# Kernel tuning notes

Hardware: AMD Instinct MI355X
Metric: run time of the kernel (lower is better)

Reference implementation:

```python
import jax, jax.numpy as jnp
import numpy as np

VOCAB = 50257
EMB = 512


def setup_inputs() -> dict:
    key = jax.random.key(0)
    k1, k2, k3 = jax.random.split(key, 3)
    input_token_ids = jax.random.randint(k1, (8, 4096), 0, VOCAB, dtype=jnp.int64 if jax.config.jax_enable_x64 else jnp.int32)
    W = jax.random.normal(k2, (EMB, VOCAB), dtype=jnp.float32)  # nn.Linear(vocab, emb).weight
    b = jax.random.normal(k3, (EMB,), dtype=jnp.float32)        # nn.Linear bias
    return {"input_token_ids": input_token_ids, "W": W, "b": b}


def reference(input_token_ids, W, b):
    # one_hot(ids, V) @ W.T + b  ==  W.T[ids] + b   (exact same math, gather form)
    scale = jnp.asarray(EMB, W.dtype) ** 0.5
    emb = jnp.take(W.T, input_token_ids, axis=0)  # [B, S, EMB]
    return (emb + b) * scale
```

## Files before the change

kernel.cpp:

```cpp
#include <hip/hip_runtime.h>


constexpr int VOCAB = 50257;
constexpr int EMB   = 512;
constexpr int NTOK  = 8 * 4096;
constexpr float SCALE = 22.62741699796952f;

constexpr int VB   = 64;
constexpr int NB   = (VOCAB + VB - 1) / VB;
constexpr int CAP  = 96;
constexpr int ESPL = 4;
constexpr int RWV  = 32;
constexpr int RS   = VB + 1;


__global__ __launch_bounds__(256) void build_buckets(
    const int* __restrict__ ids,
    int* __restrict__ counts,
    int* __restrict__ olist,
    int* __restrict__ buckets)
{
    int t = blockIdx.x * 256 + threadIdx.x;
    int id = ids[t];
    int bkt = id >> 6;
    int slot = atomicAdd(&counts[bkt], 1);
    if (slot < CAP) {
        buckets[bkt * CAP + slot] = (t << 6) | (id & 63);
    } else {
        int o = atomicAdd(&counts[NB], 1);
        olist[o] = t;
    }
}

__global__ __launch_bounds__(256) void scatter_main(
    const float* __restrict__ W,
    const float* __restrict__ bias,
    const int*   __restrict__ counts,
    const int*   __restrict__ buckets,
    const int*   __restrict__ olist,
    const int*   __restrict__ ids,
    float*       __restrict__ out)
{
    __shared__ float tile[4][RWV * RS];
    __shared__ int   toks[CAP];
    __shared__ int   s_cnt;

    const int bid  = blockIdx.x;
    const int b    = bid >> 2;
    const int z    = bid & 3;
    const int tid  = threadIdx.x;
    const int lane = tid & 63;
    const int w    = tid >> 6;

    if (tid == 0) s_cnt = counts[b];
    if (tid < CAP) toks[tid] = buckets[b * CAP + tid];
    __syncthreads();
    const int cnt = min(s_cnt, CAP);

    const int e0 = z * 128 + w * RWV;
    const int el = lane & 31;
    const float be = bias[e0 + el];

    const int v = b * VB + lane;
    const float* wsrc = W + (v < VOCAB ? v : VOCAB - 1);

    if (cnt > 0) {
        #pragma unroll
        for (int r = 0; r < RWV; ++r) {
            const float* gp = wsrc + (size_t)(e0 + r) * VOCAB;
            float* lp = &tile[w][r * RS];
            __builtin_amdgcn_global_load_lds(
                (const __attribute__((address_space(1))) void*)gp,
                (__attribute__((address_space(3))) void*)lp, 4, 0, 0);
        }
        asm volatile("s_waitcnt vmcnt(0)" ::: "memory");

        const int half = lane >> 5;
        const float* tw = &tile[w][el * RS];
        for (int i = 0; i < cnt; i += 2) {
            int j  = i + half;
            int jj = j < cnt ? j : cnt - 1;
            int pk = toks[jj];
            int t  = pk >> 6;
            int vl = pk & 63;
            float val = (tw[vl] + be) * SCALE;
            if (j < cnt) out[(size_t)t * EMB + e0 + el] = val;
        }
    }

    if (b == 0) {
        int n = counts[NB];
        for (int ww = w; ww < n; ww += 4) {
            int t  = olist[ww];
            int id = ids[t];
            #pragma unroll
            for (int m = 0; m < 2; ++m) {
                int e = z * 128 + lane + m * 64;
                out[(size_t)t * EMB + e] = (W[(size_t)e * VOCAB + id] + bias[e]) * SCALE;
            }
        }
    }
}

__global__ __launch_bounds__(256) void embed_gather(
    const int*   __restrict__ ids,
    const float* __restrict__ W,
    const float* __restrict__ b,
    float*       __restrict__ out)
{
    int idx4 = blockIdx.x * blockDim.x + threadIdx.x;
    int t    = idx4 >> 7;
    int e    = (idx4 & 127) << 2;
    int id = ids[t];
    float4 bb = *reinterpret_cast<const float4*>(b + e);
    const float* wcol = W + (size_t)id;
    float4 o;
    o.x = (wcol[(size_t)(e + 0) * VOCAB] + bb.x) * SCALE;
    o.y = (wcol[(size_t)(e + 1) * VOCAB] + bb.y) * SCALE;
    o.z = (wcol[(size_t)(e + 2) * VOCAB] + bb.z) * SCALE;
    o.w = (wcol[(size_t)(e + 3) * VOCAB] + bb.w) * SCALE;
    *reinterpret_cast<float4*>(out + (size_t)idx4 * 4) = o;
}

extern "C" void kernel_launch(void* const* d_in, const int* in_sizes, int n_in,
                              void* d_out, int out_size, void* d_ws, size_t ws_size,
                              hipStream_t stream)
{
    const int*   ids  = (const int*)  d_in[0];
    const float* W    = (const float*)d_in[1];
    const float* bias = (const float*)d_in[2];
    float*       out  = (float*)d_out;

    const size_t ws_ints_needed = (size_t)NB + 1 + NTOK + (size_t)NB * CAP;

    if (ws_size >= ws_ints_needed * sizeof(int)) {
        int* counts  = (int*)d_ws;
        int* olist   = counts + NB + 1;
        int* buckets = olist + NTOK;

        hipMemsetAsync(counts, 0, (NB + 1) * sizeof(int), stream);
        build_buckets<<<NTOK / 256, 256, 0, stream>>>(ids, counts, olist, buckets);
        scatter_main<<<NB * ESPL, 256, 0, stream>>>(W, bias, counts, buckets,
                                                    olist, ids, out);
    } else {
        constexpr int total4 = NTOK * EMB / 4;
        embed_gather<<<total4 / 256, 256, 0, stream>>>(ids, W, bias, out);
    }
}
```

Before: 195.9 us.

## Use 16-byte swizzled LDS loads and register-held token lists in scatter kernel

Rewrites the W tile staging in scatter_main to use 16-byte global_load_lds transfers from 4-aligned row segments into an XOR-swizzled LDS layout, plus a small tail buffer for the misaligned remainder. The per-block token list now lives in registers and is broadcast with readlane instead of going through shared memory and a __syncthreads. The output loop is unrolled four-wide so loads are batched before stores. This targets fewer load instructions and less sync overhead, at the cost of more complex and fragile indexing (alignment, vadj for the last bucket, and the tail path).

After: 196.4 us. No clear change (+0.3%).

```diff
diff --git a/kernel.cpp b/kernel.cpp
--- a/kernel.cpp
+++ b/kernel.cpp
@@ -11,7 +11,8 @@
 constexpr int CAP  = 96;
 constexpr int ESPL = 4;
 constexpr int RWV  = 32;
-constexpr int RS   = VB + 1;
+constexpr int MAIN_DW = RWV * 64;
+constexpr int TAIL_DW = RWV * 4;
 
 
 __global__ __launch_bounds__(256) void build_buckets(
@@ -41,9 +42,7 @@
     const int*   __restrict__ ids,
     float*       __restrict__ out)
 {
-    __shared__ float tile[4][RWV * RS];
-    __shared__ int   toks[CAP];
-    __shared__ int   s_cnt;
+    __shared__ float tile[4][MAIN_DW + TAIL_DW];
 
     const int bid  = blockIdx.x;
     const int b    = bid >> 2;
@@ -52,40 +51,78 @@
     const int lane = tid & 63;
     const int w    = tid >> 6;
 
-    if (tid == 0) s_cnt = counts[b];
-    if (tid < CAP) toks[tid] = buckets[b * CAP + tid];
-    __syncthreads();
-    const int cnt = min(s_cnt, CAP);
+    const int e0     = z * 128 + w * RWV;
+    const int vstart = min(b * VB, VOCAB - VB);
+    const int vadj   = b * VB - vstart;
 
-    const int e0 = z * 128 + w * RWV;
-    const int el = lane & 31;
-    const float be = bias[e0 + el];
+    int   cnt_v = counts[b];
+    int   tok_a = buckets[b * CAP + lane];
+    int   tok_b = buckets[b * CAP + 64 + (lane & 31)];
+    float be    = bias[e0 + (lane & 31)];
 
-    const int v = b * VB + lane;
-    const float* wsrc = W + (v < VOCAB ? v : VOCAB - 1);
-
-    if (cnt > 0) {
+    {
+        const int rl = lane >> 4;
+        const int p  = lane & 15;
         #pragma unroll
-        for (int r = 0; r < RWV; ++r) {
-            const float* gp = wsrc + (size_t)(e0 + r) * VOCAB;
-            float* lp = &tile[w][r * RS];
+        for (int i = 0; i < 8; ++i) {
+            const int r = 4 * i + rl;
+            const int q = p ^ (r & 15);
+            const size_t rowdw = (size_t)(e0 + r) * VOCAB + vstart;
+            const float* gp = W + ((rowdw & ~(size_t)3) + 4 * (size_t)q);
+            float* lp = &tile[w][i * 256];
+            __builtin_amdgcn_global_load_lds(
+                (const __attribute__((address_space(1))) void*)gp,
+                (__attribute__((address_space(3))) void*)lp, 16, 0, 0);
+        }
+        #pragma unroll
+        for (int j = 0; j < 2; ++j) {
+            const int f = 64 * j + lane;
+            const int r = f >> 2, d = f & 3;
+            const size_t rowdw = (size_t)(e0 + r) * VOCAB + vstart;
+            const float* gp = W + (rowdw + 60 + d);
+            float* lp = &tile[w][MAIN_DW + j * 64];
             __builtin_amdgcn_global_load_lds(
                 (const __attribute__((address_space(1))) void*)gp,
                 (__attribute__((address_space(3))) void*)lp, 4, 0, 0);
         }
-        asm volatile("s_waitcnt vmcnt(0)" ::: "memory");
+    }
 
-        const int half = lane >> 5;
-        const float* tw = &tile[w][el * RS];
-        for (int i = 0; i < cnt; i += 2) {
-            int j  = i + half;
-            int jj = j < cnt ? j : cnt - 1;
-            int pk = toks[jj];
-            int t  = pk >> 6;
-            int vl = pk & 63;
-            float val = (tw[vl] + be) * SCALE;
-            if (j < cnt) out[(size_t)t * EMB + e0 + el] = val;
+    const int cnt = min(__builtin_amdgcn_readfirstlane(cnt_v), CAP);
+
+    const int half = lane >> 5;
+    const int el   = lane & 31;
+    const int m    = (el + vstart) & 3;
+    const float* tw = &tile[w][0];
+
+    asm volatile("s_waitcnt vmcnt(0)" ::: "memory");
+    __builtin_amdgcn_sched_barrier(0);
+
+    float* outp = out + e0 + el;
+
+    for (int i = 0; i < cnt; i += 8) {
+        float v[4]; int tt[4]; bool ok[4];
+        #pragma unroll
+        for (int u = 0; u < 4; ++u) {
+            const int j0 = i + 2 * u;
+            const int j1 = j0 + 1;
+            const int jc0 = j0 < cnt ? j0 : cnt - 1;
+            const int jc1 = j1 < cnt ? j1 : cnt - 1;
+            const int pk0 = (jc0 < 64) ? __builtin_amdgcn_readlane(tok_a, jc0)
+                                       : __builtin_amdgcn_readlane(tok_b, jc0 & 31);
+            const int pk1 = (jc1 < 64) ? __builtin_amdgcn_readlane(tok_a, jc1)
+                                       : __builtin_amdgcn_readlane(tok_b, jc1 & 31);
+            const int pk = half ? pk1 : pk0;
+            const int vl = (pk & 63) + vadj;
+            const int wc = vl + m;
+            const int a_main = el * 64 + ((((wc >> 2) ^ (el & 15))) << 2) + (wc & 3);
+            const int a_tail = MAIN_DW + el * 4 + (vl - 60);
+            v[u]  = tw[wc < 64 ? a_main : a_tail];
+            tt[u] = pk >> 6;
+            ok[u] = (j0 + half) < cnt;
         }
+        #pragma unroll
+        for (int u = 0; u < 4; ++u)
+            if (ok[u]) outp[(size_t)tt[u] * EMB] = (v[u] + be) * SCALE;
     }
 
     if (b == 0) {
@@ -94,8 +131,8 @@
             int t  = olist[ww];
             int id = ids[t];
             #pragma unroll
-            for (int m = 0; m < 2; ++m) {
-                int e = z * 128 + lane + m * 64;
+            for (int mm = 0; mm < 2; ++mm) {
+                int e = z * 128 + lane + mm * 64;
                 out[(size_t)t * EMB + e] = (W[(size_t)e * VOCAB + id] + bias[e]) * SCALE;
             }
         }
```

## Load W tile with aligned float4 reads into swizzled LDS instead of per-dword global_load_lds

Applied to the files above, without the earlier changes.

Replaces 32 per-dword global_load_lds instructions per wave with eight aligned float4 global loads per lane plus a small tail load, written into a swizzled LDS layout to avoid bank conflicts. The loads are issued before the barrier so they overlap the bucket/count reads, and the final partial vocab block is handled by clamping vstart and offsetting the column. The cost is more complex address arithmetic in the scatter loop, and the tile is now loaded even for buckets with zero tokens.

After: 195.1 us. About the same (-0.4%).

```diff
diff --git a/kernel.cpp b/kernel.cpp
--- a/kernel.cpp
+++ b/kernel.cpp
@@ -11,7 +11,8 @@
 constexpr int CAP  = 96;
 constexpr int ESPL = 4;
 constexpr int RWV  = 32;
-constexpr int RS   = VB + 1;
+constexpr int MAIN_DW = RWV * 64;
+constexpr int TAIL_DW = RWV * 4;
 
 
 __global__ __launch_bounds__(256) void build_buckets(
@@ -41,7 +42,7 @@
     const int*   __restrict__ ids,
     float*       __restrict__ out)
 {
-    __shared__ float tile[4][RWV * RS];
+    __shared__ float tile[4][MAIN_DW + TAIL_DW];
     __shared__ int   toks[CAP];
     __shared__ int   s_cnt;
 
@@ -52,40 +53,61 @@
     const int lane = tid & 63;
     const int w    = tid >> 6;
 
+    const int e0     = z * 128 + w * RWV;
+    const int vstart = min(b * VB, VOCAB - VB);
+    const int vadj   = b * VB - vstart;
+
     if (tid == 0) s_cnt = counts[b];
     if (tid < CAP) toks[tid] = buckets[b * CAP + tid];
+
+    const int rl = lane >> 4;
+    const int p  = lane & 15;
+    float4 m4[8];
+    #pragma unroll
+    for (int i = 0; i < 8; ++i) {
+        const int r = 4 * i + rl;
+        const size_t rowdw = (size_t)(e0 + r) * VOCAB + vstart;
+        m4[i] = *reinterpret_cast<const float4*>(
+                    W + ((rowdw & ~(size_t)3) + 4 * (size_t)p));
+    }
+    float tl0, tl1;
+    {
+        const int f0 = lane,      r0 = f0 >> 2, d0 = f0 & 3;
+        const int f1 = 64 + lane, r1 = f1 >> 2, d1 = f1 & 3;
+        tl0 = W[(size_t)(e0 + r0) * VOCAB + vstart + 60 + d0];
+        tl1 = W[(size_t)(e0 + r1) * VOCAB + vstart + 60 + d1];
+    }
+    const float be = bias[e0 + (lane & 31)];
+
+    #pragma unroll
+    for (int i = 0; i < 8; ++i) {
+        const int r = 4 * i + rl;
+        *reinterpret_cast<float4*>(
+            &tile[w][r * 64 + (((p + r) & 15) << 2)]) = m4[i];
+    }
+    tile[w][MAIN_DW + lane]      = tl0;
+    tile[w][MAIN_DW + 64 + lane] = tl1;
+
     __syncthreads();
     const int cnt = min(s_cnt, CAP);
 
-    const int e0 = z * 128 + w * RWV;
-    const int el = lane & 31;
-    const float be = bias[e0 + el];
+    const int half = lane >> 5;
+    const int el   = lane & 31;
+    const int m    = (el + vstart) & 3;
+    const float* tw = &tile[w][0];
+    float* outp = out + e0 + el;
 
-    const int v = b * VB + lane;
-    const float* wsrc = W + (v < VOCAB ? v : VOCAB - 1);
-
-    if (cnt > 0) {
-        #pragma unroll
-        for (int r = 0; r < RWV; ++r) {
-            const float* gp = wsrc + (size_t)(e0 + r) * VOCAB;
-            float* lp = &tile[w][r * RS];
-            __builtin_amdgcn_global_load_lds(
-                (const __attribute__((address_space(1))) void*)gp,
-                (__attribute__((address_space(3))) void*)lp, 4, 0, 0);
-        }
-        asm volatile("s_waitcnt vmcnt(0)" ::: "memory");
-
-        const int half = lane >> 5;
-        const float* tw = &tile[w][el * RS];
-        for (int i = 0; i < cnt; i += 2) {
-            int j  = i + half;
-            int jj = j < cnt ? j : cnt - 1;
-            int pk = toks[jj];
-            int t  = pk >> 6;
-            int vl = pk & 63;
-            float val = (tw[vl] + be) * SCALE;
-            if (j < cnt) out[(size_t)t * EMB + e0 + el] = val;
-        }
+    for (int i = 0; i < cnt; i += 2) {
+        const int j  = i + half;
+        const int jj = j < cnt ? j : cnt - 1;
+        const int pk = toks[jj];
+        const int t  = pk >> 6;
+        const int vl = (pk & 63) + vadj;
+        const int wc = vl + m;
+        const int a_main = el * 64 + ((((wc >> 2) + el) & 15) << 2) + (wc & 3);
+        const int a_tail = MAIN_DW + el * 4 + (vl - 60);
+        const float v = tw[wc < 64 ? a_main : a_tail];
+        if (j < cnt) outp[(size_t)t * EMB] = (v + be) * SCALE;
     }
 
     if (b == 0) {
@@ -94,8 +116,8 @@
             int t  = olist[ww];
             int id = ids[t];
             #pragma unroll
-            for (int m = 0; m < 2; ++m) {
-                int e = z * 128 + lane + m * 64;
+            for (int mm = 0; mm < 2; ++mm) {
+                int e = z * 128 + lane + mm * 64;
                 out[(size_t)t * EMB + e] = (W[(size_t)e * VOCAB + id] + bias[e]) * SCALE;
             }
         }
```

## Restructure scatter to full-row float4 writes with swizzled LDS tile per vocab bucket

Applied to the files above, without the earlier changes.

Halves the vocab bucket width to 32 and has each block load a full 256-element embedding chunk of W for its bucket into LDS, using an XOR swizzle to avoid bank conflicts. Output writes become float4 stores covering a contiguous 1 KB row segment per token, instead of scalar 32-float strips split across four blocks. This targets write coalescing and redundant per-block index loads. The trade-off is more blocks overall, block-wide syncs between chunks, and a larger LDS tile that may lower occupancy.

Result: faster. 188.9 us (-3.6%).

```diff
diff --git a/kernel.cpp b/kernel.cpp
--- a/kernel.cpp
+++ b/kernel.cpp
@@ -6,12 +6,11 @@
 constexpr int NTOK  = 8 * 4096;
 constexpr float SCALE = 22.62741699796952f;
 
-constexpr int VB   = 64;
+constexpr int VB   = 32;
 constexpr int NB   = (VOCAB + VB - 1) / VB;
 constexpr int CAP  = 96;
-constexpr int ESPL = 4;
-constexpr int RWV  = 32;
-constexpr int RS   = VB + 1;
+constexpr int ECH  = 256;
+constexpr int NCH  = EMB / ECH;
 
 
 __global__ __launch_bounds__(256) void build_buckets(
@@ -22,10 +21,10 @@
 {
     int t = blockIdx.x * 256 + threadIdx.x;
     int id = ids[t];
-    int bkt = id >> 6;
+    int bkt = id >> 5;
     int slot = atomicAdd(&counts[bkt], 1);
     if (slot < CAP) {
-        buckets[bkt * CAP + slot] = (t << 6) | (id & 63);
+        buckets[bkt * CAP + slot] = (t << 5) | (id & 31);
     } else {
         int o = atomicAdd(&counts[NB], 1);
         olist[o] = t;
@@ -41,51 +40,67 @@
     const int*   __restrict__ ids,
     float*       __restrict__ out)
 {
-    __shared__ float tile[4][RWV * RS];
+    __shared__ float tile[ECH * VB];
     __shared__ int   toks[CAP];
     __shared__ int   s_cnt;
 
-    const int bid  = blockIdx.x;
-    const int b    = bid >> 2;
-    const int z    = bid & 3;
+    const int b    = blockIdx.x;
     const int tid  = threadIdx.x;
     const int lane = tid & 63;
     const int w    = tid >> 6;
 
+    const int vstart = min(b * VB, VOCAB - VB);
+    const int vadj   = b * VB - vstart;
+
     if (tid == 0) s_cnt = counts[b];
     if (tid < CAP) toks[tid] = buckets[b * CAP + tid];
-    __syncthreads();
-    const int cnt = min(s_cnt, CAP);
 
-    const int e0 = z * 128 + w * RWV;
-    const int el = lane & 31;
-    const float be = bias[e0 + el];
+    const int pos  = lane & 31;
+    const int rh   = lane >> 5;
+    const int cc_s = (lane >> 1) & 31;
 
-    const int v = b * VB + lane;
-    const float* wsrc = W + (v < VOCAB ? v : VOCAB - 1);
+    float4 bb[NCH];
+    #pragma unroll
+    for (int c = 0; c < NCH; ++c)
+        bb[c] = *reinterpret_cast<const float4*>(bias + c * ECH + 4 * lane);
 
-    if (cnt > 0) {
+    int cnt = 0;
+
+    #pragma unroll
+    for (int c = 0; c < NCH; ++c) {
         #pragma unroll
-        for (int r = 0; r < RWV; ++r) {
-            const float* gp = wsrc + (size_t)(e0 + r) * VOCAB;
-            float* lp = &tile[w][r * RS];
+        for (int i = 0; i < 32; ++i) {
+            const int r = w * 64 + 2 * i + rh;
+            const int s = (r >> 3) & 31;
+            const float* gp = W + ((size_t)(c * ECH + r) * VOCAB
+                                   + (vstart + (pos ^ s)));
+            float* lp = &tile[(w * 64 + 2 * i) * VB];
             __builtin_amdgcn_global_load_lds(
                 (const __attribute__((address_space(1))) void*)gp,
                 (__attribute__((address_space(3))) void*)lp, 4, 0, 0);
         }
-        asm volatile("s_waitcnt vmcnt(0)" ::: "memory");
+        __syncthreads();
+        if (c == 0) cnt = min(s_cnt, CAP);
 
-        const int half = lane >> 5;
-        const float* tw = &tile[w][el * RS];
-        for (int i = 0; i < cnt; i += 2) {
-            int j  = i + half;
-            int jj = j < cnt ? j : cnt - 1;
-            int pk = toks[jj];
-            int t  = pk >> 6;
-            int vl = pk & 63;
-            float val = (tw[vl] + be) * SCALE;
-            if (j < cnt) out[(size_t)t * EMB + e0 + el] = val;
+        const float* tl = &tile[lane * 128];
+        const float4 bc = bb[c];
+        for (int i = w; i < cnt; i += 4) {
+            const int pk = toks[i];
+            const int t  = pk >> 5;
+            const int vl = (pk & 31) + vadj;
+            const int cc = vl ^ cc_s;
+            float4 o;
+            o.x = tl[      cc];
+            o.y = tl[ 32 + cc];
+            o.z = tl[ 64 + cc];
+            o.w = tl[ 96 + cc];
+            o.x = (o.x + bc.x) * SCALE;
+            o.y = (o.y + bc.y) * SCALE;
+            o.z = (o.z + bc.z) * SCALE;
+            o.w = (o.w + bc.w) * SCALE;
+            *reinterpret_cast<float4*>(out + (size_t)t * EMB + c * ECH + 4 * lane) = o;
         }
+        if (c + 1 < NCH) __syncthreads();
     }
 
     if (b == 0) {
@@ -94,8 +109,8 @@
             int t  = olist[ww];
             int id = ids[t];
             #pragma unroll
-            for (int m = 0; m < 2; ++m) {
-                int e = z * 128 + lane + m * 64;
+            for (int m = 0; m < 8; ++m) {
+                int e = lane + m * 64;
                 out[(size_t)t * EMB + e] = (W[(size_t)e * VOCAB + id] + bias[e]) * SCALE;
             }
         }
@@ -140,8 +155,8 @@
 
         hipMemsetAsync(counts, 0, (NB + 1) * sizeof(int), stream);
         build_buckets<<<NTOK / 256, 256, 0, stream>>>(ids, counts, olist, buckets);
-        scatter_main<<<NB * ESPL, 256, 0, stream>>>(W, bias, counts, buckets,
-                                                    olist, ids, out);
+        scatter_main<<<NB, 256, 0, stream>>>(W, bias, counts, buckets,
+                                             olist, ids, out);
     } else {
         constexpr int total4 = NTOK * EMB / 4;
         embed_gather<<<total4 / 256, 256, 0, stream>>>(ids, W, bias, out);
```
